# Kernel tuning notes

Measured on AMD Instinct MI355X. Metric: run time of the kernel, lower is better.

The kernel has to match this reference:

```python
import jax, jax.numpy as jnp
import numpy as np

B, C, HS, WS = 4, 256, 64, 64
E, NH, TOPK, MLP = 256, 8, 512, 1024
HD = E // NH
CHUNK = 16   # chunk size over random-query subset for L1 cdist
EPS = 1e-5


def setup_inputs() -> dict:
    key = jax.random.key(0)
    ks = jax.random.split(key, 8)
    s = 0.02
    return {
        "query_source": jax.random.normal(ks[0], (B, C, HS, WS), jnp.float32),
        "context": jax.random.normal(ks[1], (B, C, HS, WS), jnp.float32),
        "rand_token_ind": jax.random.randint(ks[2], (B, TOPK), 0, HS * WS),
        "in_proj_w": jax.random.normal(ks[3], (3 * E, E), jnp.float32) * s,
        "in_proj_b": jnp.zeros((3 * E,), jnp.float32),
        "out_proj_w": jax.random.normal(ks[4], (E, E), jnp.float32) * s,
        "out_proj_b": jnp.zeros((E,), jnp.float32),
        "conv1_w": jax.random.normal(ks[5], (MLP, C), jnp.float32) * s,
        "conv1_b": jnp.zeros((MLP,), jnp.float32),
        "bn1_gamma": jnp.ones((MLP,), jnp.float32),
        "bn1_beta": jnp.zeros((MLP,), jnp.float32),
        "bn1_mean": jnp.zeros((MLP,), jnp.float32),
        "bn1_var": jnp.ones((MLP,), jnp.float32),
        "conv2_w": jax.random.normal(ks[6], (C, MLP), jnp.float32) * s,
        "conv2_b": jnp.zeros((C,), jnp.float32),
        "bn2_gamma": jnp.ones((C,), jnp.float32),
        "bn2_beta": jnp.zeros((C,), jnp.float32),
        "bn2_mean": jnp.zeros((C,), jnp.float32),
        "bn2_var": jnp.ones((C,), jnp.float32),
    }


def _min_l1_dist(K, Qs):
    """min over random-query subset of L1 distances. K:[B,Lkv,D], Qs:[B,tk,D] -> [B,Lkv].
    Chunked scan over tk to avoid materializing [B,Lkv,tk,D]."""
    b, tk, d = Qs.shape
    nc = tk // CHUNK
    Qc = Qs.reshape(b, nc, CHUNK, d).transpose(1, 0, 2, 3)  # [nc,B,CHUNK,D]
    init = jnp.full(K.shape[:2], jnp.inf, K.dtype)

    def step(carry, q):
        dist = jnp.abs(K[:, :, None, :] - q[:, None, :, :]).sum(-1)  # [B,Lkv,CHUNK]
        return jnp.minimum(carry, dist.min(-1)), None

    md, _ = jax.lax.scan(step, init, Qc)
    return md


def _forward(query_source, context, rand_token_ind, in_proj_w, in_proj_b,
             out_proj_w, out_proj_b, conv1_w, conv1_b, bn1_gamma, bn1_beta,
             bn1_mean, bn1_var, conv2_w, conv2_b, bn2_gamma, bn2_beta,
             bn2_mean, bn2_var):
    b, c, h, w = query_source.shape
    q_tok = query_source.reshape(b, c, -1).transpose(0, 2, 1)   # [B,Lq,E]
    kv_tok = context.reshape(b, c, -1).transpose(0, 2, 1)       # [B,Lkv,E]

    # --- dist_to_random_Q_selection (top_k < Lkv) ---
    Qs = jnp.take_along_axis(q_tok, rand_token_ind[:, :, None], axis=1)  # [B,tk,E]
    md = _min_l1_dist(kv_tok, Qs)                                        # [B,Lkv]
    idx = jnp.argsort(md, axis=1)[:, :TOPK]                              # smallest, sorted
    k_sel = jnp.take_along_axis(kv_tok, idx[:, :, None], axis=1)         # [B,TOPK,E]
    v_sel = k_sel                                                        # keys==values==context

    # --- nn.MultiheadAttention (eval, batch_first) ---
    wq, wk, wv = in_proj_w[:E], in_proj_w[E:2 * E], in_proj_w[2 * E:]
    bq, bk, bv = in_proj_b[:E], in_proj_b[E:2 * E], in_proj_b[2 * E:]
    q = (q_tok @ wq.T + bq).reshape(b, -1, NH, HD)
    k = (k_sel @ wk.T + bk).reshape(b, TOPK, NH, HD)
    v = (v_sel @ wv.T + bv).reshape(b, TOPK, NH, HD)
    scores = jnp.einsum('bqhd,bkhd->bhqk', q, k) / jnp.sqrt(jnp.float32(HD))
    attn = jax.nn.softmax(scores, axis=-1)
    ctx = jnp.einsum('bhqk,bkhd->bqhd', attn, v).reshape(b, -1, E)
    out = ctx @ out_proj_w.T + out_proj_b                               # [B,Lq,E]
    attn_out = out.transpose(0, 2, 1).reshape(b, c, h, w)

    # --- residual conv MLP (1x1 convs, batchnorm eval) ---
    def conv1x1(x, wgt, bias):
        return jnp.einsum('bchw,oc->bohw', x, wgt) + bias[None, :, None, None]

    def bn(x, g, bt, m, v_):
        inv = g / jnp.sqrt(v_ + EPS)
        return x * inv[None, :, None, None] + (bt - m * inv)[None, :, None, None]

    hdn = jax.nn.relu(bn(conv1x1(attn_out, conv1_w, conv1_b),
                         bn1_gamma, bn1_beta, bn1_mean, bn1_var))
    y = bn(conv1x1(hdn, conv2_w, conv2_b), bn2_gamma, bn2_beta, bn2_mean, bn2_var)
    return attn_out + y


def reference(query_source, context, rand_token_ind, in_proj_w, in_proj_b,
              out_proj_w, out_proj_b, conv1_w, conv1_b, bn1_gamma, bn1_beta,
              bn1_mean, bn1_var, conv2_w, conv2_b, bn2_gamma, bn2_beta,
              bn2_mean, bn2_var):
    return _forward(query_source, context, rand_token_ind, in_proj_w, in_proj_b,
                    out_proj_w, out_proj_b, conv1_w, conv1_b, bn1_gamma, bn1_beta,
                    bn1_mean, bn1_var, conv2_w, conv2_b, bn2_gamma, bn2_beta,
                    bn2_mean, bn2_var)
```

## Files before the change

### kernel.cpp

```cpp
#include <hip/hip_runtime.h>
#include <math.h>

#define B_ 4
#define C_ 256
#define L_ 4096
#define E_ 256
#define NH_ 8
#define HD_ 32
#define TOPK_ 512
#define MLP_ 1024
#define EPS_ 1e-5f

#if __has_attribute(amdgpu_agpr_alloc)
#define NO_AGPR __attribute__((amdgpu_agpr_alloc(0)))
#else
#define NO_AGPR
#endif

typedef __attribute__((ext_vector_type(4))) float f32x4;
typedef __attribute__((ext_vector_type(8))) short short8;
typedef __attribute__((ext_vector_type(2))) unsigned int u32x2;
typedef __attribute__((ext_vector_type(4))) unsigned int u32x4;

#define GLOAD_LDS(srcp, ldsp)                                                                     \
  __builtin_amdgcn_global_load_lds((const __attribute__((address_space(1))) void*)(srcp),         \
                                   (__attribute__((address_space(3))) void*)(ldsp), 16, 0, 0)

__device__ __forceinline__ unsigned short f2bf(float x) {
  unsigned u = __float_as_uint(x);
  return (unsigned short)((u + 0x7FFFu + ((u >> 16) & 1)) >> 16);
}
__device__ __forceinline__ float bf2f(unsigned short h) { return __uint_as_float((unsigned)h << 16); }

__device__ __forceinline__ float dpp_red16(float s) {
  s += __int_as_float(__builtin_amdgcn_update_dpp(0, __float_as_int(s), 0x121, 0xF, 0xF, false));
  s += __int_as_float(__builtin_amdgcn_update_dpp(0, __float_as_int(s), 0x122, 0xF, 0xF, false));
  s += __int_as_float(__builtin_amdgcn_update_dpp(0, __float_as_int(s), 0x124, 0xF, 0xF, false));
  s += __int_as_float(__builtin_amdgcn_update_dpp(0, __float_as_int(s), 0x128, 0xF, 0xF, false));
  return s;
}

__device__ __forceinline__ void conv_bf8(const float* __restrict__ W, unsigned short* __restrict__ D, int blk,
                                         int tid) {
  int i = (blk * 256 + tid) * 8;
  float4 x = *(const float4*)(W + i);
  float4 y = *(const float4*)(W + i + 4);
  u32x4 w;
  w.x = (unsigned)f2bf(x.x) | ((unsigned)f2bf(x.y) << 16);
  w.y = (unsigned)f2bf(x.z) | ((unsigned)f2bf(x.w) << 16);
  w.z = (unsigned)f2bf(y.x) | ((unsigned)f2bf(y.y) << 16);
  w.w = (unsigned)f2bf(y.z) | ((unsigned)f2bf(y.w) << 16);
  *(u32x4*)(D + i) = w;
}

__global__ __launch_bounds__(256) void k_setup(const float* __restrict__ ipw, const float* __restrict__ opw,
                                               const float* __restrict__ c1w, const float* __restrict__ c2w,
                                               const float* __restrict__ qs_in, const float* __restrict__ ctx_in,
                                               unsigned short* __restrict__ wq_bf, unsigned short* __restrict__ wkv_bf,
                                               unsigned short* __restrict__ c1w_bf, unsigned short* __restrict__ c2w_bf,
                                               unsigned short* __restrict__ opw_d, unsigned* __restrict__ md,
                                               float* __restrict__ Qt, unsigned short* __restrict__ Qt_bf,
                                               float* __restrict__ Kt) {
  __shared__ float tile[32][33];
  const int bx = blockIdx.x;
  const int tid = threadIdx.x;
  if (bx < 480) {
    if (bx < 32) {
      conv_bf8(ipw, wq_bf, bx, tid);
    } else if (bx < 96) {
      conv_bf8(ipw + 65536, wkv_bf, bx - 32, tid);
    } else if (bx < 224) {
      conv_bf8(c1w, c1w_bf, bx - 96, tid);
    } else if (bx < 352) {
      conv_bf8(c2w, c2w_bf, bx - 224, tid);
    } else if (bx < 416) {
      int i = ((bx - 352) * 256 + tid) * 4;
      int k = i & 255;
      int n = i >> 8;
      float4 x = *(const float4*)(opw + i);
      unsigned short h0 = f2bf(x.x), h1 = f2bf(x.y), h2 = f2bf(x.z), h3 = f2bf(x.w);
      unsigned short l0 = f2bf(x.x - bf2f(h0)), l1 = f2bf(x.y - bf2f(h1));
      unsigned short l2 = f2bf(x.z - bf2f(h2)), l3 = f2bf(x.w - bf2f(h3));
      u32x2 hv, lv;
      hv.x = (unsigned)h0 | ((unsigned)h1 << 16); hv.y = (unsigned)h2 | ((unsigned)h3 << 16);
      lv.x = (unsigned)l0 | ((unsigned)l1 << 16); lv.y = (unsigned)l2 | ((unsigned)l3 << 16);
      unsigned short* dst = opw_d + (long)n * 512 + (k >> 5) * 64 + (k & 31);
      *(u32x2*)dst = hv;
      *(u32x2*)(dst + 32) = lv;
    } else {
      md[(bx - 416) * 256 + tid] = 0x7f800000u;
    }
    return;
  }
  int tb = bx - 480;
  const float* in;
  float* out;
  unsigned short* outbf;
  int wbf;
  if (tb < 4096) {
    in = qs_in; out = Qt; outbf = Qt_bf; wbf = 1;
  } else {
    tb -= 4096; in = ctx_in; out = Kt; outbf = nullptr; wbf = 0;
  }
  const int x = tb & 127, y = (tb >> 7) & 7, b = tb >> 10;
  const int l0 = x * 32, c0 = y * 32;
  const int tx = tid & 31, ty = tid >> 5;
  const float* ib = in + (long)b * C_ * L_;
  float* ob = out + (long)b * L_ * C_;
#pragma unroll
  for (int i = ty; i < 32; i += 8) tile[i][tx] = ib[(long)(c0 + i) * L_ + l0 + tx];
  __syncthreads();
#pragma unroll
  for (int i = ty; i < 32; i += 8) {
    float v = tile[tx][i];
    long off = (long)(l0 + i) * C_ + c0 + tx;
    ob[off] = v;
    if (wbf) outbf[(long)b * L_ * C_ + off] = f2bf(v);
  }
}

__global__ __launch_bounds__(256) void k_gather_f32(const float* __restrict__ src, const int* __restrict__ ind,
                                                    float* __restrict__ dst, int nrows) {
  int gr = blockIdx.x * 4 + (threadIdx.x >> 6);
  int b = gr / nrows, r = gr % nrows;
  int c = (threadIdx.x & 63) * 4;
  int idx = ind[b * nrows + r];
  *(float4*)(dst + ((long)b * nrows + r) * C_ + c) = *(const float4*)(src + ((long)b * L_ + idx) * C_ + c);
}

__global__ __launch_bounds__(256) void k_gather_bf(const float* __restrict__ src, const int* __restrict__ ind,
                                                   unsigned short* __restrict__ dst, int nrows) {
  int gr = blockIdx.x * 4 + (threadIdx.x >> 6);
  int b = gr / nrows, r = gr % nrows;
  int c = (threadIdx.x & 63) * 4;
  int idx = ind[b * nrows + r];
  float4 x = *(const float4*)(src + ((long)b * L_ + idx) * C_ + c);
  u32x2 w;
  w.x = (unsigned)f2bf(x.x) | ((unsigned)f2bf(x.y) << 16);
  w.y = (unsigned)f2bf(x.z) | ((unsigned)f2bf(x.w) << 16);
  *(u32x2*)(dst + ((long)b * nrows + r) * C_ + c) = w;
}

__global__ __launch_bounds__(256) NO_AGPR void k_dist(const float* __restrict__ Kt, const float* __restrict__ Qs,
                                                      unsigned* __restrict__ mdbits) {
  __shared__ float Kl[16 * 256];
  __shared__ unsigned mdl[64];
  const int b = blockIdx.y, tb = blockIdx.x, qz = blockIdx.z;
  const int tid = threadIdx.x;
  const int cg = tid & 15, qslot = tid >> 4;
  float4 Q[4][4];
  {
    const float* qbase = Qs + ((long)b * TOPK_ + qz * 64 + qslot) * C_ + cg * 4;
#pragma unroll
    for (int r = 0; r < 4; r++)
#pragma unroll
      for (int i = 0; i < 4; i++) Q[r][i] = *(const float4*)(qbase + (long)r * 16 * C_ + i * 64);
  }
#pragma unroll
  for (int r = 0; r < 4; r++) {
    asm volatile("" : "+v"(Q[r][0].x), "+v"(Q[r][0].y), "+v"(Q[r][0].z), "+v"(Q[r][0].w),
                      "+v"(Q[r][1].x), "+v"(Q[r][1].y), "+v"(Q[r][1].z), "+v"(Q[r][1].w));
    asm volatile("" : "+v"(Q[r][2].x), "+v"(Q[r][2].y), "+v"(Q[r][2].z), "+v"(Q[r][2].w),
                      "+v"(Q[r][3].x), "+v"(Q[r][3].y), "+v"(Q[r][3].z), "+v"(Q[r][3].w));
  }
  if (tid < 64) mdl[tid] = 0x7f800000u;
  for (int ck = 0; ck < 4; ck++) {
    __syncthreads();
    {
      const float4* src = (const float4*)(Kt + ((long)b * L_ + tb * 64 + ck * 16) * C_);
      float4* dst = (float4*)Kl;
#pragma unroll
      for (int j = 0; j < 4; j++) dst[tid + j * 256] = src[tid + j * 256];
    }
    __syncthreads();
    for (int t = 0; t < 16; t++) {
      const float* kp = &Kl[t * 256 + cg * 4];
      float4 k0 = *(const float4*)kp;
      float4 k1 = *(const float4*)(kp + 64);
      float4 k2 = *(const float4*)(kp + 128);
      float4 k3 = *(const float4*)(kp + 192);
      float d0, d1, d2, d3;
#define DIST_R(r, dst_)                                                                                   \
  dst_ = (((fabsf(k0.x - Q[r][0].x) + fabsf(k0.y - Q[r][0].y)) +                                          \
           (fabsf(k0.z - Q[r][0].z) + fabsf(k0.w - Q[r][0].w))) +                                         \
          ((fabsf(k1.x - Q[r][1].x) + fabsf(k1.y - Q[r][1].y)) +                                          \
           (fabsf(k1.z - Q[r][1].z) + fabsf(k1.w - Q[r][1].w)))) +                                        \
         (((fabsf(k2.x - Q[r][2].x) + fabsf(k2.y - Q[r][2].y)) +                                          \
           (fabsf(k2.z - Q[r][2].z) + fabsf(k2.w - Q[r][2].w))) +                                         \
          ((fabsf(k3.x - Q[r][3].x) + fabsf(k3.y - Q[r][3].y)) +                                          \
           (fabsf(k3.z - Q[r][3].z) + fabsf(k3.w - Q[r][3].w))))
      DIST_R(0, d0);
      DIST_R(1, d1);
      DIST_R(2, d2);
      DIST_R(3, d3);
#undef DIST_R
      d0 = dpp_red16(d0);
      d1 = dpp_red16(d1);
      d2 = dpp_red16(d2);
      d3 = dpp_red16(d3);
      float mn = fminf(fminf(d0, d1), fminf(d2, d3));
      mn = fminf(mn, __int_as_float(__builtin_amdgcn_ds_swizzle(__float_as_int(mn), 0x401F)));
      if ((tid & 31) == 0) atomicMin(&mdl[ck * 16 + t], __float_as_uint(mn));
    }
  }
  __syncthreads();
  if (tid < 64) atomicMin(&mdbits[(long)b * L_ + tb * 64 + tid], mdl[tid]);
}

__global__ __launch_bounds__(1024) void k_select(const unsigned* __restrict__ mdb, unsigned* __restrict__ idxsel) {
  __shared__ unsigned vals[4096];
  __shared__ unsigned cnts[32];
  __shared__ unsigned out_n, tie_n;
  __shared__ unsigned short ties[1024];
  const int b = blockIdx.x, tid = threadIdx.x;
  const int lane = tid & 63;
#pragma unroll
  for (int s = 0; s < 4; s++) vals[tid + s * 1024] = mdb[b * 4096 + tid + s * 1024];
  if (tid < 32) cnts[tid] = 0;
  if (tid == 0) { out_n = 0; tie_n = 0; }
  __syncthreads();
  unsigned cur = 0;
  for (int bit = 31; bit >= 0; --bit) {
    unsigned cand = cur | (1u << bit);
    int c = 0;
#pragma unroll
    for (int s = 0; s < 4; s++) {
      unsigned long long bal = __ballot(vals[tid + s * 1024] < cand);
      c += __popcll(bal);
    }
    if (lane == 0) atomicAdd(&cnts[bit], (unsigned)c);
    __syncthreads();
    if (cnts[bit] < 512u) cur = cand;
  }
  const unsigned M = cur;
#pragma unroll
  for (int s = 0; s < 4; s++) {
    int i = tid + s * 1024;
    unsigned v = vals[i];
    if (v < M) {
      unsigned p = atomicAdd(&out_n, 1u);
      idxsel[b * TOPK_ + p] = (unsigned)i;
    } else if (v == M) {
      unsigned t = atomicAdd(&tie_n, 1u);
      if (t < 1024u) ties[t] = (unsigned short)i;
    }
  }
  __syncthreads();
  if (tid == 0) {
    int n1 = (int)out_n;
    int nt = (int)tie_n; if (nt > 1024) nt = 1024;
    int need = 512 - n1; if (need > nt) need = nt;
    for (int j = 0; j < need; j++) {
      int bi = 1 << 30, best = -1;
      for (int t = 0; t < nt; t++) {
        int ix = ties[t];
        if (ix < bi) { bi = ix; best = t; }
      }
      ties[best] = 0xFFFF;
      idxsel[b * TOPK_ + n1 + j] = (unsigned)bi;
    }
  }
}

template <int BN, int MODE>
__global__ __launch_bounds__(256) void k_gemm_s(
    const unsigned short* __restrict__ A, const unsigned short* __restrict__ Bm, int K, int N, float cscale,
    const float* __restrict__ bias, const float* __restrict__ g, const float* __restrict__ be,
    const float* __restrict__ mu, const float* __restrict__ va, const float* __restrict__ Xres,
    float* __restrict__ Cf, unsigned short* __restrict__ Cb, unsigned short* __restrict__ Caux) {
  constexpr int NWN = (BN == 128) ? 2 : 1;
  constexpr int WR = (NWN == 2) ? 64 : 32;
  constexpr int MG = WR / 16, NG = 4;
  __shared__ __align__(16) unsigned short As[128 * 64];
  __shared__ __align__(16) unsigned short Bs[BN * 64];
  const int tid = threadIdx.x;
  const int wid = tid >> 6, lane = tid & 63, lr = lane & 15, lg = lane >> 4;
  const int wm = wid / NWN, wn = wid % NWN;
  const int row0 = wm * WR, col0 = wn * 64;
  char* AsB = (char*)As;
  char* BsB = (char*)Bs;
  f32x4 acc[MG][NG];
#pragma unroll
  for (int m = 0; m < MG; m++)
#pragma unroll
    for (int n = 0; n < NG; n++) acc[m][n] = (f32x4){0.f, 0.f, 0.f, 0.f};

  for (int k0 = 0; k0 < K; k0 += 64) {
    if (k0) __syncthreads();
    {
#pragma unroll
      for (int j = 0; j < 4; j++) {
        int gix = j * 256 + tid;
        int r = gix >> 3, s = gix & 7;
        int csrc = s ^ (r & 7);
        const unsigned short* srcp = A + (long)(blockIdx.y * 128 + r) * K + k0 + csrc * 8;
        GLOAD_LDS(srcp, AsB + gix * 16);
      }
    }
    if (BN == 128) {
#pragma unroll
      for (int j = 0; j < 4; j++) {
        int gix = j * 256 + tid;
        int r = gix >> 3, s = gix & 7;
        int csrc = s ^ (r & 7);
        const unsigned short* srcp = Bm + (long)(blockIdx.x * 128 + r) * K + k0 + csrc * 8;
        GLOAD_LDS(srcp, BsB + gix * 16);
      }
    } else {
#pragma unroll
      for (int j = 0; j < 2; j++) {
        int gix = j * 256 + tid;
        int r = gix >> 3, s = gix & 7;
        int csrc = s ^ (r & 7);
        const unsigned short* srcp = Bm + (long)(blockIdx.x * 64 + r) * K + k0 + csrc * 8;
        GLOAD_LDS(srcp, BsB + gix * 16);
      }
    }
    __syncthreads();
    short8 a0[MG], a1[MG], b0[NG], b1[NG];
#pragma unroll
    for (int m = 0; m < MG; m++) {
      int rr = row0 + m * 16 + lr;
      a0[m] = *(const short8*)(AsB + rr * 128 + (((0 + lg) ^ (rr & 7)) << 4));
      a1[m] = *(const short8*)(AsB + rr * 128 + (((4 + lg) ^ (rr & 7)) << 4));
    }
#pragma unroll
    for (int n = 0; n < NG; n++) {
      int rr = col0 + n * 16 + lr;
      b0[n] = *(const short8*)(BsB + rr * 128 + (((0 + lg) ^ (rr & 7)) << 4));
      b1[n] = *(const short8*)(BsB + rr * 128 + (((4 + lg) ^ (rr & 7)) << 4));
    }
#pragma unroll
    for (int m = 0; m < MG; m++)
#pragma unroll
      for (int n = 0; n < NG; n++)
        acc[m][n] = __builtin_amdgcn_mfma_f32_16x16x32_bf16(a0[m], b0[n], acc[m][n], 0, 0, 0);
#pragma unroll
    for (int m = 0; m < MG; m++)
#pragma unroll
      for (int n = 0; n < NG; n++)
        acc[m][n] = __builtin_amdgcn_mfma_f32_16x16x32_bf16(a1[m], b1[n], acc[m][n], 0, 0, 0);
  }
  const int mbase = blockIdx.y * 128 + row0 + lg * 4;
  const int nbase = blockIdx.x * BN + col0;
#pragma unroll
  for (int n = 0; n < NG; n++) {
    int nn = nbase + n * 16 + lr;
    float bb = bias[nn];
    float inv = 0.f, sh = 0.f;
    if (MODE == 3 || MODE == 5) {
      inv = g[nn] / sqrtf(va[nn] + EPS_);
      sh = be[nn] - mu[nn] * inv;
    }
#pragma unroll
    for (int m = 0; m < MG; m++) {
#pragma unroll
      for (int r = 0; r < 4; r++) {
        int mm = mbase + m * 16 + r;
        float v = acc[m][n][r] + bb;
        if (MODE == 0) {
          Cb[(long)mm * N + nn] = f2bf(v * cscale);
        } else if (MODE == 1) {
          if (nn < 256) {
            Cb[(long)mm * 256 + nn] = f2bf(v);
          } else {
            int bi = mm >> 9, t = mm & 511;
            Caux[((long)bi * 256 + (nn - 256)) * 512 + t] = f2bf(v);
          }
        } else if (MODE == 3) {
          v = v * inv + sh;
          v = fmaxf(v, 0.f);
          Cb[(long)mm * N + nn] = f2bf(v);
        } else if (MODE == 5) {
          v = v * inv + sh + Xres[(long)mm * 256 + nn];
          int bi = mm >> 12, l = mm & 4095;
          Cf[(long)bi * (C_ * L_) + (long)nn * L_ + l] = v;
        }
      }
    }
  }
}

__global__ __launch_bounds__(256) void k_gemm_d(const unsigned short* __restrict__ A,
                                                const unsigned short* __restrict__ Bd, int K,
                                                const float* __restrict__ bias, float* __restrict__ Cf,
                                                unsigned short* __restrict__ Cb) {
  constexpr int MG = 2, NG = 4;
  __shared__ __align__(16) unsigned short As[128 * 64];
  __shared__ __align__(16) unsigned short Bs[64 * 64];
  const int tid = threadIdx.x;
  const int wid = tid >> 6, lane = tid & 63, lr = lane & 15, lg = lane >> 4;
  const int row0 = wid * 32;
  char* AsB = (char*)As;
  char* BsB = (char*)Bs;
  f32x4 acc[MG][NG];
#pragma unroll
  for (int m = 0; m < MG; m++)
#pragma unroll
    for (int n = 0; n < NG; n++) acc[m][n] = (f32x4){0.f, 0.f, 0.f, 0.f};

  for (int kb = 0; kb < K; kb += 32) {
    if (kb) __syncthreads();
    {
#pragma unroll
      for (int j = 0; j < 4; j++) {
        int gix = j * 256 + tid;
        int r = gix >> 3, s = gix & 7;
        int csrc = s ^ (r & 7);
        const unsigned short* srcp = A + (long)(blockIdx.y * 128 + r) * (2 * K) + kb * 2 + csrc * 8;
        GLOAD_LDS(srcp, AsB + gix * 16);
      }
    }
    {
#pragma unroll
      for (int j = 0; j < 2; j++) {
        int gix = j * 256 + tid;
        int r = gix >> 3, s = gix & 7;
        int csrc = s ^ (r & 7);
        const unsigned short* srcp = Bd + (long)(blockIdx.x * 64 + r) * (2 * K) + kb * 2 + csrc * 8;
        GLOAD_LDS(srcp, BsB + gix * 16);
      }
    }
    __syncthreads();
    short8 a0[MG], a1[MG], b0[NG], b1[NG];
#pragma unroll
    for (int m = 0; m < MG; m++) {
      int rr = row0 + m * 16 + lr;
      a0[m] = *(const short8*)(AsB + rr * 128 + (((0 + lg) ^ (rr & 7)) << 4));
      a1[m] = *(const short8*)(AsB + rr * 128 + (((4 + lg) ^ (rr & 7)) << 4));
    }
#pragma unroll
    for (int n = 0; n < NG; n++) {
      int rr = n * 16 + lr;
      b0[n] = *(const short8*)(BsB + rr * 128 + (((0 + lg) ^ (rr & 7)) << 4));
      b1[n] = *(const short8*)(BsB + rr * 128 + (((4 + lg) ^ (rr & 7)) << 4));
    }
#pragma unroll
    for (int m = 0; m < MG; m++)
#pragma unroll
      for (int n = 0; n < NG; n++)
        acc[m][n] = __builtin_amdgcn_mfma_f32_16x16x32_bf16(a0[m], b0[n], acc[m][n], 0, 0, 0);
#pragma unroll
    for (int m = 0; m < MG; m++)
#pragma unroll
      for (int n = 0; n < NG; n++)
        acc[m][n] = __builtin_amdgcn_mfma_f32_16x16x32_bf16(a1[m], b0[n], acc[m][n], 0, 0, 0);
#pragma unroll
    for (int m = 0; m < MG; m++)
#pragma unroll
      for (int n = 0; n < NG; n++)
        acc[m][n] = __builtin_amdgcn_mfma_f32_16x16x32_bf16(a0[m], b1[n], acc[m][n], 0, 0, 0);
  }
  const int mbase = blockIdx.y * 128 + row0 + lg * 4;
  const int nbase = blockIdx.x * 64;
#pragma unroll
  for (int n = 0; n < NG; n++) {
    int nn = nbase + n * 16 + lr;
    float bb = bias[nn];
#pragma unroll
    for (int m = 0; m < MG; m++) {
#pragma unroll
      for (int r = 0; r < 4; r++) {
        int mm = mbase + m * 16 + r;
        float v = acc[m][n][r] + bb;
        Cf[(long)mm * 256 + nn] = v;
        Cb[(long)mm * 256 + nn] = f2bf(v);
      }
    }
  }
}

__global__ __launch_bounds__(256) void k_attn_mfma(const unsigned short* __restrict__ qbf,
                                                   const unsigned short* __restrict__ kvk,
                                                   const unsigned short* __restrict__ vt,
                                                   unsigned short* __restrict__ ctxd) {
  __shared__ __align__(16) unsigned short PT[4 * 1024];
  const int tid = threadIdx.x, wid = tid >> 6, lane = tid & 63, lr = lane & 15, lg = lane >> 4;
  const int b = blockIdx.z, h = blockIdx.y;
  const int q0 = blockIdx.x * 64 + wid * 16;
  char* pt = (char*)(PT + wid * 1024);
  short8 qf = *(const short8*)(qbf + ((long)(b * L_ + q0 + lr)) * E_ + h * HD_ + lg * 8);
  f32x4 o0 = (f32x4){0.f, 0.f, 0.f, 0.f}, o1 = (f32x4){0.f, 0.f, 0.f, 0.f};
  float lsum = 0.f;
  for (int t0 = 0; t0 < TOPK_; t0 += 64) {
    f32x4 sc[4];
#pragma unroll
    for (int f = 0; f < 4; f++) {
      short8 kf = *(const short8*)(kvk + ((long)(b * TOPK_ + t0 + f * 16 + lr)) * E_ + h * HD_ + lg * 8);
      f32x4 z = (f32x4){0.f, 0.f, 0.f, 0.f};
      sc[f] = __builtin_amdgcn_mfma_f32_16x16x32_bf16(kf, qf, z, 0, 0, 0);
    }
    float csum = 0.f;
#pragma unroll
    for (int f = 0; f < 4; f++) {
      float e0 = __expf(sc[f][0]), e1 = __expf(sc[f][1]), e2 = __expf(sc[f][2]), e3 = __expf(sc[f][3]);
      csum += (e0 + e1) + (e2 + e3);
      u32x2 w;
      w.x = (unsigned)f2bf(e0) | ((unsigned)f2bf(e1) << 16);
      w.y = (unsigned)f2bf(e2) | ((unsigned)f2bf(e3) << 16);
      *(u32x2*)(pt + lr * 128 + ((((f * 2 + (lg >> 1)) ^ (lr & 7))) << 4) + (lg & 1) * 8) = w;
    }
    csum += __shfl_xor(csum, 16);
    csum += __shfl_xor(csum, 32);
    lsum += csum;
#pragma unroll
    for (int ks = 0; ks < 2; ks++) {
      short8 pf = *(const short8*)(pt + lr * 128 + (((ks * 4 + lg) ^ (lr & 7)) << 4));
      {
        short8 vf = *(const short8*)(vt + ((long)(b * 256 + h * HD_ + 0 + lr)) * 512 + t0 + ks * 32 + lg * 8);
        o0 = __builtin_amdgcn_mfma_f32_16x16x32_bf16(pf, vf, o0, 0, 0, 0);
      }
      {
        short8 vf = *(const short8*)(vt + ((long)(b * 256 + h * HD_ + 16 + lr)) * 512 + t0 + ks * 32 + lg * 8);
        o1 = __builtin_amdgcn_mfma_f32_16x16x32_bf16(pf, vf, o1, 0, 0, 0);
      }
    }
  }
#pragma unroll
  for (int r = 0; r < 4; r++) {
    float li = 1.0f / __shfl(lsum, lg * 4 + r);
    long base = ((long)(b * L_ + q0 + lg * 4 + r)) * 512 + h * 64;
    float v0 = o0[r] * li, v1 = o1[r] * li;
    unsigned short h0 = f2bf(v0), h1 = f2bf(v1);
    ctxd[base + lr] = h0;
    ctxd[base + 32 + lr] = f2bf(v0 - bf2f(h0));
    ctxd[base + 16 + lr] = h1;
    ctxd[base + 48 + lr] = f2bf(v1 - bf2f(h1));
  }
}

extern "C" void kernel_launch(void* const* d_in, const int* in_sizes, int n_in, void* d_out, int out_size, void* d_ws,
                              size_t ws_size, hipStream_t stream) {
  (void)in_sizes; (void)n_in; (void)out_size; (void)ws_size;
  const float* qs_in = (const float*)d_in[0];
  const float* ctx_in = (const float*)d_in[1];
  const int* rind = (const int*)d_in[2];
  const float* ipw = (const float*)d_in[3];
  const float* ipb = (const float*)d_in[4];
  const float* opw = (const float*)d_in[5];
  const float* opb = (const float*)d_in[6];
  const float* c1w = (const float*)d_in[7];
  const float* c1b = (const float*)d_in[8];
  const float* g1 = (const float*)d_in[9];
  const float* b1 = (const float*)d_in[10];
  const float* mu1 = (const float*)d_in[11];
  const float* v1 = (const float*)d_in[12];
  const float* c2w = (const float*)d_in[13];
  const float* c2b = (const float*)d_in[14];
  const float* g2 = (const float*)d_in[15];
  const float* b2 = (const float*)d_in[16];
  const float* mu2 = (const float*)d_in[17];
  const float* v2 = (const float*)d_in[18];
  float* out = (float*)d_out;
  float* ws = (float*)d_ws;

  float* Qt = ws;
  unsigned short* ctxd = (unsigned short*)ws;
  float* Kt = ws + 4194304;
  float* X = ws + 4194304;
  unsigned short* Qt_bf = (unsigned short*)(ws + 8388608);
  unsigned short* X_bf = (unsigned short*)(ws + 8388608);
  float* Qsbuf = ws + 10485760;
  unsigned* md = (unsigned*)(ws + 11010048);
  unsigned* idxsel = (unsigned*)(ws + 11026432);
  unsigned short* ksel_bf = (unsigned short*)(ws + 11272192);
  unsigned short* q_bf = (unsigned short*)(ws + 11534336);
  unsigned short* kv_k = (unsigned short*)(ws + 13631488);
  unsigned short* v_t = (unsigned short*)(ws + 13893632);
  unsigned short* H = (unsigned short*)(ws + 10485760);
  unsigned short* wq_bf = (unsigned short*)(ws + 18874368);
  unsigned short* wkv_bf = (unsigned short*)(ws + 18907136);
  unsigned short* c1w_bf = (unsigned short*)(ws + 18972672);
  unsigned short* c2w_bf = (unsigned short*)(ws + 19103744);
  unsigned short* opw_d = (unsigned short*)(ws + 19234816);

  const float qscale = 0.17677669529663687f;

  k_setup<<<8672, 256, 0, stream>>>(ipw, opw, c1w, c2w, qs_in, ctx_in, wq_bf, wkv_bf, c1w_bf, c2w_bf, opw_d, md, Qt,
                                    Qt_bf, Kt);
  k_gather_f32<<<512, 256, 0, stream>>>(Qt, rind, Qsbuf, TOPK_);
  k_dist<<<dim3(64, 4, 8), 256, 0, stream>>>(Kt, Qsbuf, md);
  k_select<<<4, 1024, 0, stream>>>(md, idxsel);
  k_gather_bf<<<512, 256, 0, stream>>>(Kt, (const int*)idxsel, ksel_bf, TOPK_);

  k_gemm_s<64, 0><<<dim3(4, 128), 256, 0, stream>>>(Qt_bf, wq_bf, 256, 256, qscale, ipb, nullptr, nullptr, nullptr,
                                                    nullptr, nullptr, nullptr, q_bf, nullptr);
  k_gemm_s<64, 1><<<dim3(8, 16), 256, 0, stream>>>(ksel_bf, wkv_bf, 256, 512, 1.f, ipb + 256, nullptr, nullptr,
                                                   nullptr, nullptr, nullptr, nullptr, kv_k, v_t);
  k_attn_mfma<<<dim3(64, NH_, B_), 256, 0, stream>>>(q_bf, kv_k, v_t, ctxd);
  k_gemm_d<<<dim3(4, 128), 256, 0, stream>>>(ctxd, opw_d, 256, opb, X, X_bf);
  k_gemm_s<128, 3><<<dim3(8, 128), 256, 0, stream>>>(X_bf, c1w_bf, 256, 1024, 1.f, c1b, g1, b1, mu1, v1, nullptr,
                                                     nullptr, H, nullptr);
  k_gemm_s<64, 5><<<dim3(4, 128), 256, 0, stream>>>(H, c2w_bf, 1024, 256, 1.f, c2b, g2, b2, mu2, v2, X, out,
                                                    nullptr, nullptr);
}
```

Before: 280.0 us.

## Fuse Q-projection GEMM into distance kernel and gather queries inside setup

Drops the fp32 transposed copy of the query source. The random query rows are now gathered directly from the NCHW input inside the setup kernel, which removes the separate gather launch. The Q projection GEMM moves into extra blocks of the L1-distance kernel so the two independent stages run in one launch and share the GPU. The cost is strided uncoalesced reads in the new gather, a larger shared-memory footprint for the distance blocks, and removal of the no-AGPR attribute, which may change register allocation.

```diff
diff --git a/kernel.cpp b/kernel.cpp
--- a/kernel.cpp
+++ b/kernel.cpp
@@ -10,12 +10,6 @@
 #define TOPK_ 512
 #define MLP_ 1024
 #define EPS_ 1e-5f
-
-#if __has_attribute(amdgpu_agpr_alloc)
-#define NO_AGPR __attribute__((amdgpu_agpr_alloc(0)))
-#else
-#define NO_AGPR
-#endif
 
 typedef __attribute__((ext_vector_type(4))) float f32x4;
 typedef __attribute__((ext_vector_type(8))) short short8;
@@ -56,11 +50,12 @@
 __global__ __launch_bounds__(256) void k_setup(const float* __restrict__ ipw, const float* __restrict__ opw,
                                                const float* __restrict__ c1w, const float* __restrict__ c2w,
                                                const float* __restrict__ qs_in, const float* __restrict__ ctx_in,
+                                               const int* __restrict__ rind,
                                                unsigned short* __restrict__ wq_bf, unsigned short* __restrict__ wkv_bf,
                                                unsigned short* __restrict__ c1w_bf, unsigned short* __restrict__ c2w_bf,
                                                unsigned short* __restrict__ opw_d, unsigned* __restrict__ md,
-                                               float* __restrict__ Qt, unsigned short* __restrict__ Qt_bf,
-                                               float* __restrict__ Kt) {
+                                               unsigned short* __restrict__ Qt_bf, float* __restrict__ Kt,
+                                               float* __restrict__ Qsbuf) {
   __shared__ float tile[32][33];
   const int bx = blockIdx.x;
   const int tid = threadIdx.x;
@@ -92,13 +87,24 @@
     }
     return;
   }
+  if (bx >= 8672) {
+    int gr = (bx - 8672) * 4 + (tid >> 6);
+    int b = gr >> 9, r = gr & 511;
+    int idx = rind[b * TOPK_ + r];
+    int c0 = (tid & 63) * 4;
+    float* dst = Qsbuf + ((long)b * TOPK_ + r) * C_ + c0;
+    const float* src = qs_in + (long)b * C_ * L_ + idx;
+#pragma unroll
+    for (int i = 0; i < 4; i++) dst[i] = src[(long)(c0 + i) * L_];
+    return;
+  }
   int tb = bx - 480;
   const float* in;
   float* out;
   unsigned short* outbf;
   int wbf;
   if (tb < 4096) {
-    in = qs_in; out = Qt; outbf = Qt_bf; wbf = 1;
+    in = qs_in; out = nullptr; outbf = Qt_bf; wbf = 1;
   } else {
     tb -= 4096; in = ctx_in; out = Kt; outbf = nullptr; wbf = 0;
   }
@@ -106,7 +112,6 @@
   const int l0 = x * 32, c0 = y * 32;
   const int tx = tid & 31, ty = tid >> 5;
   const float* ib = in + (long)b * C_ * L_;
-  float* ob = out + (long)b * L_ * C_;
 #pragma unroll
   for (int i = ty; i < 32; i += 8) tile[i][tx] = ib[(long)(c0 + i) * L_ + l0 + tx];
   __syncthreads();
@@ -114,18 +119,9 @@
   for (int i = ty; i < 32; i += 8) {
     float v = tile[tx][i];
     long off = (long)(l0 + i) * C_ + c0 + tx;
-    ob[off] = v;
     if (wbf) outbf[(long)b * L_ * C_ + off] = f2bf(v);
-  }
-}
-
-__global__ __launch_bounds__(256) void k_gather_f32(const float* __restrict__ src, const int* __restrict__ ind,
-                                                    float* __restrict__ dst, int nrows) {
-  int gr = blockIdx.x * 4 + (threadIdx.x >> 6);
-  int b = gr / nrows, r = gr % nrows;
-  int c = (threadIdx.x & 63) * 4;
-  int idx = ind[b * nrows + r];
-  *(float4*)(dst + ((long)b * nrows + r) * C_ + c) = *(const float4*)(src + ((long)b * L_ + idx) * C_ + c);
+    else out[(long)b * L_ * C_ + off] = v;
+  }
 }
 
 __global__ __launch_bounds__(256) void k_gather_bf(const float* __restrict__ src, const int* __restrict__ ind,
@@ -141,12 +137,87 @@
   *(u32x2*)(dst + ((long)b * nrows + r) * C_ + c) = w;
 }
 
-__global__ __launch_bounds__(256) NO_AGPR void k_dist(const float* __restrict__ Kt, const float* __restrict__ Qs,
-                                                      unsigned* __restrict__ mdbits) {
-  __shared__ float Kl[16 * 256];
-  __shared__ unsigned mdl[64];
-  const int b = blockIdx.y, tb = blockIdx.x, qz = blockIdx.z;
+__global__ __launch_bounds__(256) void k_dist_qp(const float* __restrict__ Kt, const float* __restrict__ Qs,
+                                                 unsigned* __restrict__ mdbits,
+                                                 const unsigned short* __restrict__ Aq,
+                                                 const unsigned short* __restrict__ Bw,
+                                                 unsigned short* __restrict__ q_bf,
+                                                 const float* __restrict__ bias, float cscale) {
+  __shared__ __align__(16) char smem[24832];
   const int tid = threadIdx.x;
+  if (blockIdx.x < 512) {
+    char* AsB = smem;
+    char* BsB = smem + 16384;
+    const int bxx = blockIdx.x;
+    const int bx_n = bxx & 3, by_m = bxx >> 2;
+    const int wid = tid >> 6, lane = tid & 63, lr = lane & 15, lg = lane >> 4;
+    const int row0 = wid * 32;
+    f32x4 acc[2][4];
+#pragma unroll
+    for (int m = 0; m < 2; m++)
+#pragma unroll
+      for (int n = 0; n < 4; n++) acc[m][n] = (f32x4){0.f, 0.f, 0.f, 0.f};
+    for (int k0 = 0; k0 < 256; k0 += 64) {
+      if (k0) __syncthreads();
+#pragma unroll
+      for (int j = 0; j < 4; j++) {
+        int gix = j * 256 + tid;
+        int r = gix >> 3, s = gix & 7;
+        int csrc = s ^ (r & 7);
+        GLOAD_LDS(Aq + (long)(by_m * 128 + r) * 256 + k0 + csrc * 8, AsB + gix * 16);
+      }
+#pragma unroll
+      for (int j = 0; j < 2; j++) {
+        int gix = j * 256 + tid;
+        int r = gix >> 3, s = gix & 7;
+        int csrc = s ^ (r & 7);
+        GLOAD_LDS(Bw + (long)(bx_n * 64 + r) * 256 + k0 + csrc * 8, BsB + gix * 16);
+      }
+      __syncthreads();
+      short8 a0[2], a1[2], b0[4], b1[4];
+#pragma unroll
+      for (int m = 0; m < 2; m++) {
+        int rr = row0 + m * 16 + lr;
+        a0[m] = *(const short8*)(AsB + rr * 128 + (((0 + lg) ^ (rr & 7)) << 4));
+        a1[m] = *(const short8*)(AsB + rr * 128 + (((4 + lg) ^ (rr & 7)) << 4));
+      }
+#pragma unroll
+      for (int n = 0; n < 4; n++) {
+        int rr = n * 16 + lr;
+        b0[n] = *(const short8*)(BsB + rr * 128 + (((0 + lg) ^ (rr & 7)) << 4));
+        b1[n] = *(const short8*)(BsB + rr * 128 + (((4 + lg) ^ (rr & 7)) << 4));
+      }
+#pragma unroll
+      for (int m = 0; m < 2; m++)
+#pragma unroll
+        for (int n = 0; n < 4; n++)
+          acc[m][n] = __builtin_amdgcn_mfma_f32_16x16x32_bf16(a0[m], b0[n], acc[m][n], 0, 0, 0);
+#pragma unroll
+      for (int m = 0; m < 2; m++)
+#pragma unroll
+        for (int n = 0; n < 4; n++)
+          acc[m][n] = __builtin_amdgcn_mfma_f32_16x16x32_bf16(a1[m], b1[n], acc[m][n], 0, 0, 0);
+    }
+    const int mbase = by_m * 128 + row0 + lg * 4;
+    const int nbase = bx_n * 64;
+#pragma unroll
+    for (int n = 0; n < 4; n++) {
+      int nn = nbase + n * 16 + lr;
+      float bb = bias[nn];
+#pragma unroll
+      for (int m = 0; m < 2; m++)
+#pragma unroll
+        for (int r = 0; r < 4; r++) {
+          int mm = mbase + m * 16 + r;
+          q_bf[(long)mm * 256 + nn] = f2bf((acc[m][n][r] + bb) * cscale);
+        }
+    }
+    return;
+  }
+  const int bxd = blockIdx.x - 512;
+  float* Kl = (float*)smem;
+  unsigned* mdl = (unsigned*)(smem + 24576);
+  const int tb = bxd & 63, b = (bxd >> 6) & 3, qz = bxd >> 8;
   const int cg = tid & 15, qslot = tid >> 4;
   float4 Q[4][4];
   {
@@ -358,9 +429,7 @@
       for (int r = 0; r < 4; r++) {
         int mm = mbase + m * 16 + r;
         float v = acc[m][n][r] + bb;
-        if (MODE == 0) {
-          Cb[(long)mm * N + nn] = f2bf(v * cscale);
-        } else if (MODE == 1) {
+        if (MODE == 1) {
           if (nn < 256) {
             Cb[(long)mm * 256 + nn] = f2bf(v);
           } else {
@@ -554,7 +623,6 @@
   float* out = (float*)d_out;
   float* ws = (float*)d_ws;
 
-  float* Qt = ws;
   unsigned short* ctxd = (unsigned short*)ws;
   float* Kt = ws + 4194304;
   float* X = ws + 4194304;
@@ -576,15 +644,11 @@
 
   const float qscale = 0.17677669529663687f;
 
-  k_setup<<<8672, 256, 0, stream>>>(ipw, opw, c1w, c2w, qs_in, ctx_in, wq_bf, wkv_bf, c1w_bf, c2w_bf, opw_d, md, Qt,
-                                    Qt_bf, Kt);
-  k_gather_f32<<<512, 256, 0, stream>>>(Qt, rind, Qsbuf, TOPK_);
-  k_dist<<<dim3(64, 4, 8), 256, 0, stream>>>(Kt, Qsbuf, md);
+  k_setup<<<9184, 256, 0, stream>>>(ipw, opw, c1w, c2w, qs_in, ctx_in, rind, wq_bf, wkv_bf, c1w_bf, c2w_bf, opw_d,
+                                    md, Qt_bf, Kt, Qsbuf);
+  k_dist_qp<<<2560, 256, 0, stream>>>(Kt, Qsbuf, md, Qt_bf, wq_bf, q_bf, ipb, qscale);
   k_select<<<4, 1024, 0, stream>>>(md, idxsel);
   k_gather_bf<<<512, 256, 0, stream>>>(Kt, (const int*)idxsel, ksel_bf, TOPK_);
-
-  k_gemm_s<64, 0><<<dim3(4, 128), 256, 0, stream>>>(Qt_bf, wq_bf, 256, 256, qscale, ipb, nullptr, nullptr, nullptr,
-                                                    nullptr, nullptr, nullptr, q_bf, nullptr);
   k_gemm_s<64, 1><<<dim3(8, 16), 256, 0, stream>>>(ksel_bf, wkv_bf, 256, 512, 1.f, ipb + 256, nullptr, nullptr,
                                                    nullptr, nullptr, nullptr, nullptr, kv_k, v_t);
   k_attn_mfma<<<dim3(64, NH_, B_), 256, 0, stream>>>(q_bf, kv_k, v_t, ctxd);
```

Result: slower. 294.8 us (+5.3%).
